# Optimization experiments

Measured on AMD Instinct MI355X. Metric: run time of the kernel, lower is better.

## Reference

```python
import jax, jax.numpy as jnp
import numpy as np

N = 50000      # total nodes (50 graphs x 1000 nodes)
G = 50         # number of graphs in the batch
NODE = 1000    # nodes per graph
E = 320000     # total edges (within-graph)
IN = 128
H1, H2 = 64, 128
HEADS = 4
NEG = 0.2      # LeakyReLU negative slope


def setup_inputs() -> dict:
    key = jax.random.key(0)
    ks = jax.random.split(key, 16)
    x = jax.random.normal(ks[0], (N, IN), jnp.float32)
    # edges confined to their own graph: per-graph offsets
    off = (jnp.arange(E) // (E // G)) * NODE
    src = jax.random.randint(ks[1], (E,), 0, NODE) + off
    dst = jax.random.randint(ks[2], (E,), 0, NODE) + off
    node2graph = jnp.arange(N) // NODE

    def lin(k, fan_in, fan_out):
        s = 1.0 / np.sqrt(fan_in)
        kw, kb = jax.random.split(k)
        return (jax.random.uniform(kw, (fan_in, fan_out), jnp.float32, -s, s),
                jax.random.uniform(kb, (fan_out,), jnp.float32, -s, s))

    W_src1, b_src1 = lin(ks[3], IN, HEADS * H1)
    W_dst1, b_dst1 = lin(ks[4], IN, HEADS * H1)
    attn1 = jax.random.normal(ks[5], (HEADS, H1), jnp.float32) * (1.0 / np.sqrt(H1))
    W_src2, b_src2 = lin(ks[6], H1, HEADS * H2)
    W_dst2, b_dst2 = lin(ks[7], H1, HEADS * H2)
    attn2 = jax.random.normal(ks[8], (HEADS, H2), jnp.float32) * (1.0 / np.sqrt(H2))
    gate_w, gate_b = lin(ks[9], H2, 1)
    return dict(x=x, src=src, dst=dst, node2graph=node2graph,
                W_src1=W_src1, b_src1=b_src1, W_dst1=W_dst1, b_dst1=b_dst1, attn1=attn1,
                W_src2=W_src2, b_src2=b_src2, W_dst2=W_dst2, b_dst2=b_dst2, attn2=attn2,
                gate_w=gate_w, gate_b=gate_b)


def gatv2_layer(h, src, dst, W_src, b_src, W_dst, b_dst, attn):
    # DGL GATv2Conv: e_ij = a^T LeakyReLU(W_src h_j + W_dst h_i), edge softmax over dst
    H, D = attn.shape
    fs = (h @ W_src + b_src).reshape(-1, H, D)  # [N,H,D]
    fd = (h @ W_dst + b_dst).reshape(-1, H, D)
    e = jax.nn.leaky_relu(fs[src] + fd[dst], NEG)        # [E,H,D]
    logits = jnp.einsum('ehd,hd->eh', e, attn)           # [E,H]
    m = jax.ops.segment_max(logits, dst, num_segments=h.shape[0])
    ex = jnp.exp(logits - m[dst])
    denom = jax.ops.segment_sum(ex, dst, num_segments=h.shape[0])
    alpha = ex / denom[dst]                              # [E,H]
    out = jax.ops.segment_sum(alpha[:, :, None] * fs[src], dst,
                              num_segments=h.shape[0])   # [N,H,D]
    return out


def reference(x, src, dst, node2graph,
              W_src1, b_src1, W_dst1, b_dst1, attn1,
              W_src2, b_src2, W_dst2, b_dst2, attn2,
              gate_w, gate_b):
    # layer 1 + head-wise maxpool -> [N, H1]
    h = gatv2_layer(x, src, dst, W_src1, b_src1, W_dst1, b_dst1, attn1).max(axis=1)
    # layer 2 + head-wise maxpool -> [N, H2]
    h = gatv2_layer(h, src, dst, W_src2, b_src2, W_dst2, b_dst2, attn2).max(axis=1)
    # global attention pooling: softmax(gate) over nodes per graph, weighted sum
    gate = h @ gate_w + gate_b                           # [N,1]
    gm = jax.ops.segment_max(gate, node2graph, num_segments=G)
    ge = jnp.exp(gate - gm[node2graph])
    gs = jax.ops.segment_sum(ge, node2graph, num_segments=G)
    alpha = ge / gs[node2graph]                          # [N,1]
    return jax.ops.segment_sum(alpha * h, node2graph, num_segments=G)  # [G, H2]
```

## Files before the change

### kernel.cpp

```cpp
#include <hip/hip_runtime.h>
#include <math.h>

#define NN 50000
#define GG 50
#define NODE 1000
#define EE 320000
#define HEADS 4

typedef __attribute__((ext_vector_type(8))) short short8;
typedef __attribute__((ext_vector_type(8))) __bf16 bf16x8;
typedef __attribute__((ext_vector_type(4))) float f32x4;

__device__ __forceinline__ unsigned short f2bf(float f) {
    unsigned int u = __float_as_uint(f);
    u = (u + 0x7fffu + ((u >> 16) & 1u)) >> 16;
    return (unsigned short)u;
}
__device__ __forceinline__ float bf2f(unsigned short s) {
    return __uint_as_float(((unsigned int)s) << 16);
}

__global__ void cvt_f32_bf16(const float* __restrict__ in, unsigned short* __restrict__ outp, int n4) {
    int i = blockIdx.x * 256 + threadIdx.x;
    if (i < n4) {
        float4 f = *(const float4*)(in + (size_t)i * 4);
        ushort4 o;
        o.x = f2bf(f.x); o.y = f2bf(f.y); o.z = f2bf(f.z); o.w = f2bf(f.w);
        *(ushort4*)(outp + (size_t)i * 4) = o;
    }
}

__global__ void wt_cvt(const float* __restrict__ W, unsigned short* __restrict__ Wt, int K, int N_) {
    int i = blockIdx.x * 256 + threadIdx.x;
    if (i < K * N_) {
        int n = i / K, k = i - n * K;
        Wt[i] = f2bf(W[(size_t)k * N_ + n]);
    }
}

__global__ void count_deg(const int* __restrict__ dst, int* __restrict__ deg, int E_) {
    int i = blockIdx.x * 256 + threadIdx.x;
    if (i < E_) atomicAdd(&deg[dst[i]], 1);
}

__global__ void scan1(const int* __restrict__ deg, int* __restrict__ bsum, int Nn) {
    __shared__ int sh[256];
    int i = blockIdx.x * 256 + threadIdx.x;
    sh[threadIdx.x] = (i < Nn) ? deg[i] : 0;
    __syncthreads();
    for (int s = 128; s > 0; s >>= 1) {
        if (threadIdx.x < s) sh[threadIdx.x] += sh[threadIdx.x + s];
        __syncthreads();
    }
    if (threadIdx.x == 0) bsum[blockIdx.x] = sh[0];
}

__global__ void scan2(int* __restrict__ bsum, int nb, int* __restrict__ rowptr, int Nn, int E_) {
    if (threadIdx.x == 0 && blockIdx.x == 0) {
        int acc = 0;
        for (int i = 0; i < nb; ++i) { int v = bsum[i]; bsum[i] = acc; acc += v; }
        rowptr[Nn] = E_;
    }
}

__global__ void scan3(const int* __restrict__ deg, const int* __restrict__ bsum,
                      int* __restrict__ rowptr, int* __restrict__ cursor, int Nn) {
    __shared__ int sh[256];
    int i = blockIdx.x * 256 + threadIdx.x;
    int v = (i < Nn) ? deg[i] : 0;
    sh[threadIdx.x] = v;
    __syncthreads();
    for (int s = 1; s < 256; s <<= 1) {
        int t = (threadIdx.x >= s) ? sh[threadIdx.x - s] : 0;
        __syncthreads();
        sh[threadIdx.x] += t;
        __syncthreads();
    }
    if (i < Nn) {
        int ex = sh[threadIdx.x] - v + bsum[blockIdx.x];
        rowptr[i] = ex;
        cursor[i] = ex;
    }
}

__global__ void scatter_edges(const int* __restrict__ src, const int* __restrict__ dst,
                              int* __restrict__ cursor, int* __restrict__ csrc, int E_) {
    int i = blockIdx.x * 256 + threadIdx.x;
    if (i < E_) { int pos = atomicAdd(&cursor[dst[i]], 1); csrc[pos] = src[i]; }
}

template<int K>
__global__ __launch_bounds__(256)
void gemm_mfma(const unsigned short* __restrict__ A, const unsigned short* __restrict__ Wt,
               const float* __restrict__ bias, unsigned short* __restrict__ C,
               int M, int Ncols) {
    __shared__ short A_lds[128 * K];
    __shared__ short B_lds[128 * K];
    constexpr int CH = K / 8;
    constexpr int ROWB = K * 2;
    int tid = threadIdx.x;
    int lane = tid & 63, wave = tid >> 6;
    int row0 = blockIdx.y * 128, col0 = blockIdx.x * 128;

    for (int c = tid; c < 128 * CH; c += 256) {
        int r = c / CH, kc = c - r * CH;
        int gr = row0 + r; if (gr >= M) gr = M - 1;
        short8 v = *(const short8*)(A + (size_t)gr * K + kc * 8);
        *(short8*)((char*)A_lds + r * ROWB + ((kc * 16) ^ ((r & 7) << 4))) = v;
    }
    for (int c = tid; c < 128 * CH; c += 256) {
        int r = c / CH, kc = c - r * CH;
        short8 v = *(const short8*)(Wt + (size_t)(col0 + r) * K + kc * 8);
        *(short8*)((char*)B_lds + r * ROWB + ((kc * 16) ^ ((r & 7) << 4))) = v;
    }
    __syncthreads();

    int wr = wave >> 1, wc = wave & 1;
    f32x4 acc[4][4] = {};
    #pragma unroll
    for (int ks = 0; ks < K / 32; ++ks) {
        int kbyte = ks * 64 + ((lane >> 4) << 4);
        short8 a[4], b[4];
        #pragma unroll
        for (int m = 0; m < 4; ++m) {
            int r = wr * 64 + m * 16 + (lane & 15);
            a[m] = *(const short8*)((const char*)A_lds + r * ROWB + (kbyte ^ ((r & 7) << 4)));
        }
        #pragma unroll
        for (int n = 0; n < 4; ++n) {
            int r = wc * 64 + n * 16 + (lane & 15);
            b[n] = *(const short8*)((const char*)B_lds + r * ROWB + (kbyte ^ ((r & 7) << 4)));
        }
        #pragma unroll
        for (int m = 0; m < 4; ++m)
            #pragma unroll
            for (int n = 0; n < 4; ++n)
                acc[m][n] = __builtin_amdgcn_mfma_f32_16x16x32_bf16(
                    __builtin_bit_cast(bf16x8, a[m]), __builtin_bit_cast(bf16x8, b[n]),
                    acc[m][n], 0, 0, 0);
    }

    #pragma unroll
    for (int m = 0; m < 4; ++m) {
        int grb = row0 + wr * 64 + m * 16 + ((lane >> 4) << 2);
        #pragma unroll
        for (int q = 0; q < 4; ++q) {
            int gr = grb + q;
            if (gr < M) {
                #pragma unroll
                for (int n = 0; n < 4; ++n) {
                    int gc = col0 + wc * 64 + n * 16 + (lane & 15);
                    C[(size_t)gr * Ncols + gc] = f2bf(acc[m][n][q] + bias[gc]);
                }
            }
        }
    }
}

template<int D>
__global__ void gat_fused(const int* __restrict__ rowptr, const int* __restrict__ csrc,
                          const unsigned short* __restrict__ fs, const unsigned short* __restrict__ fd,
                          const float* __restrict__ attn, void* __restrict__ hout, int Nn) {
    int lane = threadIdx.x & 63;
    int wave = (blockIdx.x * blockDim.x + threadIdx.x) >> 6;
    int nw = (gridDim.x * blockDim.x) >> 6;
    constexpr int VE = D / 16;
    constexpr int HD = HEADS * D;
    int head = lane >> 4;
    int doff = (lane & 15) * VE;

    float at[VE];
    #pragma unroll
    for (int j = 0; j < VE; ++j) at[j] = attn[head * D + doff + j];

    for (int n = wave; n < Nn; n += nw) {
        int b = rowptr[n], e_ = rowptr[n + 1];
        float r[VE];
        if (b == e_) {
            #pragma unroll
            for (int k = 0; k < VE; ++k) r[k] = 0.f;
        } else {
            float fdf[VE];
            if constexpr (VE == 4) {
                ushort4 vd = *(const ushort4*)(fd + (size_t)n * HD + lane * 4);
                fdf[0] = bf2f(vd.x); fdf[1] = bf2f(vd.y); fdf[2] = bf2f(vd.z); fdf[3] = bf2f(vd.w);
            } else {
                short8 vd = *(const short8*)(fd + (size_t)n * HD + lane * 8);
                #pragma unroll
                for (int k = 0; k < 8; ++k) fdf[k] = bf2f((unsigned short)vd[k]);
            }
            float m = -INFINITY, l = 0.f;
            float acc[VE];
            #pragma unroll
            for (int k = 0; k < VE; ++k) acc[k] = 0.f;

            for (int j = b; j < e_; ++j) {
                int s = csrc[j];
                float fsf[VE];
                if constexpr (VE == 4) {
                    ushort4 vs = *(const ushort4*)(fs + (size_t)s * HD + lane * 4);
                    fsf[0] = bf2f(vs.x); fsf[1] = bf2f(vs.y); fsf[2] = bf2f(vs.z); fsf[3] = bf2f(vs.w);
                } else {
                    short8 vs = *(const short8*)(fs + (size_t)s * HD + lane * 8);
                    #pragma unroll
                    for (int k = 0; k < 8; ++k) fsf[k] = bf2f((unsigned short)vs[k]);
                }
                float p = 0.f;
                #pragma unroll
                for (int k = 0; k < VE; ++k) {
                    float v = fsf[k] + fdf[k];
                    v = v >= 0.f ? v : 0.2f * v;
                    p += v * at[k];
                }
                p += __shfl_xor(p, 1);
                p += __shfl_xor(p, 2);
                p += __shfl_xor(p, 4);
                p += __shfl_xor(p, 8);
                float mn = fmaxf(m, p);
                float sc = __expf(m - mn);
                float pw = __expf(p - mn);
                l = l * sc + pw;
                #pragma unroll
                for (int k = 0; k < VE; ++k) acc[k] = acc[k] * sc + pw * fsf[k];
                m = mn;
            }
            float inv = 1.f / l;
            #pragma unroll
            for (int k = 0; k < VE; ++k) r[k] = acc[k] * inv;
        }
        #pragma unroll
        for (int k = 0; k < VE; ++k) {
            r[k] = fmaxf(r[k], __shfl_xor(r[k], 16));
            r[k] = fmaxf(r[k], __shfl_xor(r[k], 32));
        }
        if (lane < 16) {
            if constexpr (VE == 4) {
                ushort4 o;
                o.x = f2bf(r[0]); o.y = f2bf(r[1]); o.z = f2bf(r[2]); o.w = f2bf(r[3]);
                *(ushort4*)((unsigned short*)hout + (size_t)n * 64 + doff) = o;
            } else {
                float* hp = (float*)hout + (size_t)n * 128 + doff;
                *(float4*)hp = make_float4(r[0], r[1], r[2], r[3]);
                *(float4*)(hp + 4) = make_float4(r[4], r[5], r[6], r[7]);
            }
        }
    }
}

__global__ void pool_kernel(const float* __restrict__ h2, const float* __restrict__ gate_w,
                            const float* __restrict__ gate_b, float* __restrict__ out) {
    __shared__ float gate[NODE];
    __shared__ float red[256];
    int g = blockIdx.x;
    int tid = threadIdx.x;
    const float* hb = h2 + (size_t)g * NODE * 128;
    float gb = gate_b[0];
    for (int n = tid; n < NODE; n += 256) {
        const float* r = hb + (size_t)n * 128;
        float acc = 0.f;
        #pragma unroll 8
        for (int k = 0; k < 128; ++k) acc += r[k] * gate_w[k];
        gate[n] = acc + gb;
    }
    __syncthreads();
    float m = -INFINITY;
    for (int n = tid; n < NODE; n += 256) m = fmaxf(m, gate[n]);
    red[tid] = m;
    __syncthreads();
    for (int s = 128; s > 0; s >>= 1) {
        if (tid < s) red[tid] = fmaxf(red[tid], red[tid + s]);
        __syncthreads();
    }
    m = red[0];
    __syncthreads();
    float ssum = 0.f;
    for (int n = tid; n < NODE; n += 256) {
        float e = __expf(gate[n] - m);
        gate[n] = e;
        ssum += e;
    }
    red[tid] = ssum;
    __syncthreads();
    for (int s = 128; s > 0; s >>= 1) {
        if (tid < s) red[tid] += red[tid + s];
        __syncthreads();
    }
    float inv = 1.f / red[0];
    __syncthreads();
    if (tid < 128) {
        float acc = 0.f;
        for (int n = 0; n < NODE; ++n) acc += gate[n] * hb[(size_t)n * 128 + tid];
        out[g * 128 + tid] = acc * inv;
    }
}

extern "C" void kernel_launch(void* const* d_in, const int* in_sizes, int n_in,
                              void* d_out, int out_size, void* d_ws, size_t ws_size,
                              hipStream_t stream) {
    const float* x      = (const float*)d_in[0];
    const int*   src    = (const int*)d_in[1];
    const int*   dst    = (const int*)d_in[2];
    const float* W_src1 = (const float*)d_in[4];
    const float* b_src1 = (const float*)d_in[5];
    const float* W_dst1 = (const float*)d_in[6];
    const float* b_dst1 = (const float*)d_in[7];
    const float* attn1  = (const float*)d_in[8];
    const float* W_src2 = (const float*)d_in[9];
    const float* b_src2 = (const float*)d_in[10];
    const float* W_dst2 = (const float*)d_in[11];
    const float* b_dst2 = (const float*)d_in[12];
    const float* attn2  = (const float*)d_in[13];
    const float* gate_w = (const float*)d_in[14];
    const float* gate_b = (const float*)d_in[15];
    float* out = (float*)d_out;

    char* p = (char*)d_ws;
    auto alloc = [&](size_t bytes) -> void* {
        void* r = (void*)p;
        p += (bytes + 255) & ~(size_t)255;
        return r;
    };
    unsigned short* fs     = (unsigned short*)alloc((size_t)NN * 512 * 2);
    unsigned short* fd     = (unsigned short*)alloc((size_t)NN * 512 * 2);
    unsigned short* h1     = (unsigned short*)alloc((size_t)NN * 64 * 2);
    float*          h2     = (float*)alloc((size_t)NN * 128 * 4);
    unsigned short* x_bf   = (unsigned short*)alloc((size_t)NN * 128 * 2);
    unsigned short* Wt1s   = (unsigned short*)alloc((size_t)128 * 256 * 2);
    unsigned short* Wt1d   = (unsigned short*)alloc((size_t)128 * 256 * 2);
    unsigned short* Wt2s   = (unsigned short*)alloc((size_t)64 * 512 * 2);
    unsigned short* Wt2d   = (unsigned short*)alloc((size_t)64 * 512 * 2);
    int*            deg    = (int*)alloc((size_t)NN * 4);
    int*            rowptr = (int*)alloc((size_t)(NN + 1) * 4);
    int*            cursor = (int*)alloc((size_t)NN * 4);
    int*            csrc   = (int*)alloc((size_t)EE * 4);
    int*            bsum   = (int*)alloc(4096);

    cvt_f32_bf16<<<(NN * 128 / 4 + 255) / 256, 256, 0, stream>>>(x, x_bf, NN * 128 / 4);
    wt_cvt<<<(128 * 256 + 255) / 256, 256, 0, stream>>>(W_src1, Wt1s, 128, 256);
    wt_cvt<<<(128 * 256 + 255) / 256, 256, 0, stream>>>(W_dst1, Wt1d, 128, 256);
    wt_cvt<<<(64 * 512 + 255) / 256, 256, 0, stream>>>(W_src2, Wt2s, 64, 512);
    wt_cvt<<<(64 * 512 + 255) / 256, 256, 0, stream>>>(W_dst2, Wt2d, 64, 512);

    hipMemsetAsync(deg, 0, (size_t)NN * 4, stream);
    count_deg<<<(EE + 255) / 256, 256, 0, stream>>>(dst, deg, EE);
    int nb = (NN + 255) / 256;
    scan1<<<nb, 256, 0, stream>>>(deg, bsum, NN);
    scan2<<<1, 64, 0, stream>>>(bsum, nb, rowptr, NN, EE);
    scan3<<<nb, 256, 0, stream>>>(deg, bsum, rowptr, cursor, NN);
    scatter_edges<<<(EE + 255) / 256, 256, 0, stream>>>(src, dst, cursor, csrc, EE);

    int rowtiles = (NN + 127) / 128;

    gemm_mfma<128><<<dim3(2, rowtiles), 256, 0, stream>>>(x_bf, Wt1s, b_src1, fs, NN, 256);
    gemm_mfma<128><<<dim3(2, rowtiles), 256, 0, stream>>>(x_bf, Wt1d, b_dst1, fd, NN, 256);
    gat_fused<64><<<2048, 256, 0, stream>>>(rowptr, csrc, fs, fd, attn1, h1, NN);

    gemm_mfma<64><<<dim3(4, rowtiles), 256, 0, stream>>>(h1, Wt2s, b_src2, fs, NN, 512);
    gemm_mfma<64><<<dim3(4, rowtiles), 256, 0, stream>>>(h1, Wt2d, b_dst2, fd, NN, 512);
    gat_fused<128><<<2048, 256, 0, stream>>>(rowptr, csrc, fs, fd, attn2, h2, NN);

    pool_kernel<<<GG, 256, 0, stream>>>(h2, gate_w, gate_b, out);
}
```

Measured before the change: 397.2 us.

## Merge prep kernels, fold scan pass, K-tile GEMM LDS, split pooling sum

```diff
diff --git a/kernel.cpp b/kernel.cpp
--- a/kernel.cpp
+++ b/kernel.cpp
@@ -20,21 +20,28 @@
     return __uint_as_float(((unsigned int)s) << 16);
 }
 
-__global__ void cvt_f32_bf16(const float* __restrict__ in, unsigned short* __restrict__ outp, int n4) {
+__global__ void prep_cvt(const float* __restrict__ x, unsigned short* __restrict__ x_bf,
+                         const float* __restrict__ W_src1, const float* __restrict__ W_dst1,
+                         unsigned short* __restrict__ Wt1s, unsigned short* __restrict__ Wt1d,
+                         const float* __restrict__ W_src2, const float* __restrict__ W_dst2,
+                         unsigned short* __restrict__ Wt2s, unsigned short* __restrict__ Wt2d) {
     int i = blockIdx.x * 256 + threadIdx.x;
+    int n4 = NN * 128 / 4;
     if (i < n4) {
-        float4 f = *(const float4*)(in + (size_t)i * 4);
+        float4 f = *(const float4*)(x + (size_t)i * 4);
         ushort4 o;
         o.x = f2bf(f.x); o.y = f2bf(f.y); o.z = f2bf(f.z); o.w = f2bf(f.w);
-        *(ushort4*)(outp + (size_t)i * 4) = o;
-    }
-}
-
-__global__ void wt_cvt(const float* __restrict__ W, unsigned short* __restrict__ Wt, int K, int N_) {
-    int i = blockIdx.x * 256 + threadIdx.x;
-    if (i < K * N_) {
-        int n = i / K, k = i - n * K;
-        Wt[i] = f2bf(W[(size_t)k * N_ + n]);
+        *(ushort4*)(x_bf + (size_t)i * 4) = o;
+    }
+    if (i < 256 * 128) {
+        int n = i >> 7, k = i & 127;
+        Wt1s[i] = f2bf(W_src1[k * 256 + n]);
+        Wt1d[i] = f2bf(W_dst1[k * 256 + n]);
+    }
+    if (i < 512 * 64) {
+        int n = i >> 6, k = i & 63;
+        Wt2s[i] = f2bf(W_src2[k * 512 + n]);
+        Wt2d[i] = f2bf(W_dst2[k * 512 + n]);
     }
 }
 
@@ -55,18 +62,22 @@
     if (threadIdx.x == 0) bsum[blockIdx.x] = sh[0];
 }
 
-__global__ void scan2(int* __restrict__ bsum, int nb, int* __restrict__ rowptr, int Nn, int E_) {
-    if (threadIdx.x == 0 && blockIdx.x == 0) {
-        int acc = 0;
-        for (int i = 0; i < nb; ++i) { int v = bsum[i]; bsum[i] = acc; acc += v; }
-        rowptr[Nn] = E_;
-    }
-}
-
 __global__ void scan3(const int* __restrict__ deg, const int* __restrict__ bsum,
-                      int* __restrict__ rowptr, int* __restrict__ cursor, int Nn) {
+                      int* __restrict__ rowptr, int* __restrict__ cursor, int Nn, int E_) {
+    __shared__ int pr[256];
     __shared__ int sh[256];
-    int i = blockIdx.x * 256 + threadIdx.x;
+    int bid = blockIdx.x;
+    int pre = 0;
+    for (int j = threadIdx.x; j < bid; j += 256) pre += bsum[j];
+    pr[threadIdx.x] = pre;
+    __syncthreads();
+    for (int s = 128; s > 0; s >>= 1) {
+        if (threadIdx.x < s) pr[threadIdx.x] += pr[threadIdx.x + s];
+        __syncthreads();
+    }
+    int base = pr[0];
+    __syncthreads();
+    int i = bid * 256 + threadIdx.x;
     int v = (i < Nn) ? deg[i] : 0;
     sh[threadIdx.x] = v;
     __syncthreads();
@@ -77,10 +88,11 @@
         __syncthreads();
     }
     if (i < Nn) {
-        int ex = sh[threadIdx.x] - v + bsum[blockIdx.x];
+        int ex = sh[threadIdx.x] - v + base;
         rowptr[i] = ex;
         cursor[i] = ex;
     }
+    if (bid == 0 && threadIdx.x == 0) rowptr[Nn] = E_;
 }
 
 __global__ void scatter_edges(const int* __restrict__ src, const int* __restrict__ dst,
@@ -94,50 +106,54 @@
 void gemm_mfma(const unsigned short* __restrict__ A, const unsigned short* __restrict__ Wt,
                const float* __restrict__ bias, unsigned short* __restrict__ C,
                int M, int Ncols) {
-    __shared__ short A_lds[128 * K];
-    __shared__ short B_lds[128 * K];
-    constexpr int CH = K / 8;
-    constexpr int ROWB = K * 2;
+    constexpr int BK = 64;
+    __shared__ short A_lds[128 * BK];
+    __shared__ short B_lds[128 * BK];
+    constexpr int CH = BK / 8;
+    constexpr int ROWB = BK * 2;
     int tid = threadIdx.x;
     int lane = tid & 63, wave = tid >> 6;
     int row0 = blockIdx.y * 128, col0 = blockIdx.x * 128;
-
-    for (int c = tid; c < 128 * CH; c += 256) {
-        int r = c / CH, kc = c - r * CH;
-        int gr = row0 + r; if (gr >= M) gr = M - 1;
-        short8 v = *(const short8*)(A + (size_t)gr * K + kc * 8);
-        *(short8*)((char*)A_lds + r * ROWB + ((kc * 16) ^ ((r & 7) << 4))) = v;
-    }
-    for (int c = tid; c < 128 * CH; c += 256) {
-        int r = c / CH, kc = c - r * CH;
-        short8 v = *(const short8*)(Wt + (size_t)(col0 + r) * K + kc * 8);
-        *(short8*)((char*)B_lds + r * ROWB + ((kc * 16) ^ ((r & 7) << 4))) = v;
-    }
-    __syncthreads();
-
     int wr = wave >> 1, wc = wave & 1;
     f32x4 acc[4][4] = {};
-    #pragma unroll
-    for (int ks = 0; ks < K / 32; ++ks) {
-        int kbyte = ks * 64 + ((lane >> 4) << 4);
-        short8 a[4], b[4];
+
+    for (int k0 = 0; k0 < K; k0 += BK) {
+        if (k0) __syncthreads();
+        for (int c = tid; c < 128 * CH; c += 256) {
+            int r = c / CH, kc = c - r * CH;
+            int gr = row0 + r; if (gr >= M) gr = M - 1;
+            short8 v = *(const short8*)(A + (size_t)gr * K + k0 + kc * 8);
+            *(short8*)((char*)A_lds + r * ROWB + ((kc * 16) ^ ((r & 7) << 4))) = v;
+        }
+        for (int c = tid; c < 128 * CH; c += 256) {
+            int r = c / CH, kc = c - r * CH;
+            short8 v = *(const short8*)(Wt + (size_t)(col0 + r) * K + k0 + kc * 8);
+            *(short8*)((char*)B_lds + r * ROWB + ((kc * 16) ^ ((r & 7) << 4))) = v;
+        }
+        __syncthreads();
+
         #pragma unroll
-        for (int m = 0; m < 4; ++m) {
-            int r = wr * 64 + m * 16 + (lane & 15);
-            a[m] = *(const short8*)((const char*)A_lds + r * ROWB + (kbyte ^ ((r & 7) << 4)));
-        }
-        #pragma unroll
-        for (int n = 0; n < 4; ++n) {
-            int r = wc * 64 + n * 16 + (lane & 15);
-            b[n] = *(const short8*)((const char*)B_lds + r * ROWB + (kbyte ^ ((r & 7) << 4)));
-        }
-        #pragma unroll
-        for (int m = 0; m < 4; ++m)
-            #pragma unroll
-            for (int n = 0; n < 4; ++n)
-                acc[m][n] = __builtin_amdgcn_mfma_f32_16x16x32_bf16(
-                    __builtin_bit_cast(bf16x8, a[m]), __builtin_bit_cast(bf16x8, b[n]),
-                    acc[m][n], 0, 0, 0);
+        for (int ks = 0; ks < BK / 32; ++ks) {
+            int kbyte = ks * 64 + ((lane >> 4) << 4);
+            short8 a[4], b[4];
+            #pragma unroll
+            for (int m = 0; m < 4; ++m) {
+                int r = wr * 64 + m * 16 + (lane & 15);
+                a[m] = *(const short8*)((const char*)A_lds + r * ROWB + (kbyte ^ ((r & 7) << 4)));
+            }
+            #pragma unroll
+            for (int n = 0; n < 4; ++n) {
+                int r = wc * 64 + n * 16 + (lane & 15);
+                b[n] = *(const short8*)((const char*)B_lds + r * ROWB + (kbyte ^ ((r & 7) << 4)));
+            }
+            #pragma unroll
+            for (int m = 0; m < 4; ++m)
+                #pragma unroll
+                for (int n = 0; n < 4; ++n)
+                    acc[m][n] = __builtin_amdgcn_mfma_f32_16x16x32_bf16(
+                        __builtin_bit_cast(bf16x8, a[m]), __builtin_bit_cast(bf16x8, b[n]),
+                        acc[m][n], 0, 0, 0);
+        }
     }
 
     #pragma unroll
@@ -287,11 +303,13 @@
     }
     float inv = 1.f / red[0];
     __syncthreads();
-    if (tid < 128) {
-        float acc = 0.f;
-        for (int n = 0; n < NODE; ++n) acc += gate[n] * hb[(size_t)n * 128 + tid];
-        out[g * 128 + tid] = acc * inv;
-    }
+    float acc = 0.f;
+    int half = tid >> 7;
+    int k = tid & 127;
+    for (int n = half * 500; n < half * 500 + 500; ++n) acc += gate[n] * hb[(size_t)n * 128 + k];
+    red[tid] = acc;
+    __syncthreads();
+    if (tid < 128) out[g * 128 + tid] = (red[tid] + red[tid + 128]) * inv;
 }
 
 extern "C" void kernel_launch(void* const* d_in, const int* in_sizes, int n_in,
@@ -335,18 +353,14 @@
     int*            csrc   = (int*)alloc((size_t)EE * 4);
     int*            bsum   = (int*)alloc(4096);
 
-    cvt_f32_bf16<<<(NN * 128 / 4 + 255) / 256, 256, 0, stream>>>(x, x_bf, NN * 128 / 4);
-    wt_cvt<<<(128 * 256 + 255) / 256, 256, 0, stream>>>(W_src1, Wt1s, 128, 256);
-    wt_cvt<<<(128 * 256 + 255) / 256, 256, 0, stream>>>(W_dst1, Wt1d, 128, 256);
-    wt_cvt<<<(64 * 512 + 255) / 256, 256, 0, stream>>>(W_src2, Wt2s, 64, 512);
-    wt_cvt<<<(64 * 512 + 255) / 256, 256, 0, stream>>>(W_dst2, Wt2d, 64, 512);
+    prep_cvt<<<(NN * 128 / 4 + 255) / 256, 256, 0, stream>>>(
+        x, x_bf, W_src1, W_dst1, Wt1s, Wt1d, W_src2, W_dst2, Wt2s, Wt2d);
 
     hipMemsetAsync(deg, 0, (size_t)NN * 4, stream);
     count_deg<<<(EE + 255) / 256, 256, 0, stream>>>(dst, deg, EE);
     int nb = (NN + 255) / 256;
     scan1<<<nb, 256, 0, stream>>>(deg, bsum, NN);
-    scan2<<<1, 64, 0, stream>>>(bsum, nb, rowptr, NN, EE);
-    scan3<<<nb, 256, 0, stream>>>(deg, bsum, rowptr, cursor, NN);
+    scan3<<<nb, 256, 0, stream>>>(deg, bsum, rowptr, cursor, NN, EE);
     scatter_edges<<<(EE + 255) / 256, 256, 0, stream>>>(src, dst, cursor, csrc, EE);
 
     int rowtiles = (NN + 127) / 128;
```

Measured after the change: 356.6 us. 1.11x faster.
